# Kernel optimization log

Hardware: AMD Instinct MI355X
Metric: run time of the kernel (lower is better)

## Reference

```python
import jax, jax.numpy as jnp
import numpy as np

B, N = 512, 4
OBS, OBSU, ID = 128, 64, 16
STATE = OBS + OBSU - ID  # 176
M1, M2, G1, A = 256, 256, 256, 16
E = 128  # hypernet_embed


def setup_inputs() -> dict:
    key = jax.random.key(0)
    ks = jax.random.split(key, 24)

    def W(k, shape):
        return jax.random.normal(k, shape, dtype=jnp.float32) * 0.05

    inp = {"input": jax.random.normal(ks[0], (B, N, OBS + OBSU), dtype=jnp.float32)}
    # layer1_hypernet: Linear(ID, 10*E)
    inp["l1_W"] = W(ks[1], (10 * E, ID)); inp["l1_b"] = W(ks[2], (10 * E,))
    # hyper_net{i}_w / hyper_net{i}_b : Linear(E, in*out) / Linear(E, out)
    inp["w1W"] = W(ks[3], (STATE * M1, E)); inp["w1b"] = W(ks[4], (STATE * M1,))
    inp["b1W"] = W(ks[5], (M1, E));        inp["b1b"] = W(ks[6], (M1,))
    inp["w2W"] = W(ks[7], (M1 * M2, E));   inp["w2b"] = W(ks[8], (M1 * M2,))
    inp["b2W"] = W(ks[9], (M2, E));        inp["b2b"] = W(ks[10], (M2,))
    inp["w3W"] = W(ks[11], (M2 * M2, E));  inp["w3b"] = W(ks[12], (M2 * M2,))
    inp["b3W"] = W(ks[13], (M2, E));       inp["b3b"] = W(ks[14], (M2,))
    inp["w4W"] = W(ks[15], (M2 * G1, E));  inp["w4b"] = W(ks[16], (M2 * G1,))
    inp["b4W"] = W(ks[17], (G1, E));       inp["b4b"] = W(ks[18], (G1,))
    inp["w5W"] = W(ks[19], (G1 * A, E));   inp["w5b"] = W(ks[20], (G1 * A,))
    inp["b5W"] = W(ks[21], (A, E));        inp["b5b"] = W(ks[22], (A,))
    return inp


def reference(input, l1_W, l1_b, w1W, w1b, b1W, b1b, w2W, w2b, b2W, b2b,
              w3W, w3b, b3W, b3b, w4W, w4b, b4W, b4b, w5W, w5b, b5W, b5b):
    b, n, d = input.shape
    BN = b * n
    ids = input[..., -ID:].reshape(BN, ID)
    x = input[..., :-ID].reshape(BN, d - ID)  # [BN, STATE]
    # layer1_hypernet: ReLU(Linear(ID -> 10E))
    h = jax.nn.relu(ids @ l1_W.T + l1_b)  # [BN, 10E]
    chunk = lambda i: h[:, i * E:(i + 1) * E]

    def layer(x, iw, ib, wW, wb, bW, bb, out_dim, act):
        # generate per-sample weight [BN, in, out] and bias [BN, out]
        Wm = (chunk(iw) @ wW.T + wb).reshape(BN, x.shape[-1], out_dim)
        bm = chunk(ib) @ bW.T + bb
        y = jnp.einsum('bs,bsm->bm', x, Wm) + bm  # batched GEMV
        return jax.nn.relu(y) if act else y

    out = layer(x,   0, 1, w1W, w1b, b1W, b1b, M1, True)
    out = layer(out, 2, 3, w2W, w2b, b2W, b2b, M2, True)
    out = layer(out, 4, 5, w3W, w3b, b3W, b3b, M2, True)
    out = layer(out, 6, 7, w4W, w4b, b4W, b4b, G1, False)  # no ReLU after layer 4
    out = layer(out, 8, 9, w5W, w5b, b5W, b5b, A, True)
    return out.reshape(b, n, A)
```

## Files before the change

### kernel.cpp

```cpp
#include <hip/hip_runtime.h>
#include <hip/hip_bf16.h>

#define E_ 128
#define NSAMP 2048

typedef __attribute__((ext_vector_type(8))) short short8;
typedef __attribute__((ext_vector_type(4))) float floatx4;

__device__ __forceinline__ ushort f2b(float f) {
    union { __hip_bfloat16 h; ushort u; } cv;
    cv.h = __float2bfloat16(f);
    return cv.u;
}

__device__ __forceinline__ void gload_lds16(const ushort* g, ushort* l) {
    __builtin_amdgcn_global_load_lds(
        (const __attribute__((address_space(1))) void*)g,
        (__attribute__((address_space(3))) void*)l, 16, 0, 0);
}

__global__ void hyper_h(const float* __restrict__ input, const float* __restrict__ l1W,
                        const float* __restrict__ l1b, float* __restrict__ h)
{
    int b = blockIdx.x / 5;
    int o = (blockIdx.x % 5) * 256 + threadIdx.x;
    const float* ids = input + (size_t)b * 192 + 176;
    const float* w = l1W + (size_t)o * 16;
    float a = l1b[o];
#pragma unroll
    for (int i = 0; i < 16; i += 4) {
        float4 wv = *(const float4*)(w + i);
        a += ids[i] * wv.x + ids[i + 1] * wv.y + ids[i + 2] * wv.z + ids[i + 3] * wv.w;
    }
    h[(size_t)b * 1280 + o] = fmaxf(a, 0.f);
}

__global__ void x0_t(const float* __restrict__ input, float* __restrict__ xT0)
{
    int idx = blockIdx.x * 256 + threadIdx.x;
    int s = idx >> 11, b = idx & 2047;
    xT0[idx] = input[(size_t)b * 192 + s];
}

__global__ void cvt_layer(const float* __restrict__ wW, const float* __restrict__ wb,
                          const float* __restrict__ bW, ushort* __restrict__ dst,
                          int S, int M)
{
    int i = (blockIdx.x * 256 + threadIdx.x) * 8;
    const int nW = S * M * E_;
    union { ushort o[8]; uint4 v; } u;
    if (i < nW) {
        float4 a = *(const float4*)(wW + i);
        float4 b = *(const float4*)(wW + i + 4);
        u.o[0] = f2b(a.x); u.o[1] = f2b(a.y); u.o[2] = f2b(a.z); u.o[3] = f2b(a.w);
        u.o[4] = f2b(b.x); u.o[5] = f2b(b.y); u.o[6] = f2b(b.z); u.o[7] = f2b(b.w);
    } else {
        int rem = i - nW;
        int slice = rem / (M * E_);
        int r2 = rem - slice * (M * E_);
        int m = r2 >> 7, e = r2 & 127;
        if (slice == 0) {
            const float* src = bW + (size_t)m * E_ + e;
            float4 a = *(const float4*)(src);
            float4 b = *(const float4*)(src + 4);
            u.o[0] = f2b(a.x); u.o[1] = f2b(a.y); u.o[2] = f2b(a.z); u.o[3] = f2b(a.w);
            u.o[4] = f2b(b.x); u.o[5] = f2b(b.y); u.o[6] = f2b(b.z); u.o[7] = f2b(b.w);
        } else {
#pragma unroll
            for (int jj = 0; jj < 8; ++jj) {
                int s = (slice - 1) * 128 + e + jj;
                u.o[jj] = (s < S) ? f2b(wb[(size_t)s * M + m]) : (ushort)0;
            }
        }
    }
    *(uint4*)(dst + i) = u.v;
}

__global__ __launch_bounds__(256, 2) void gemm_big(
    const ushort* __restrict__ wWb, const float* __restrict__ h,
    const float* __restrict__ xT, float* __restrict__ partial,
    int S, int iw, int ksplit, int btiles, int ntiles)
{
    __shared__ __align__(16) ushort Bs[2][2 * 128 * 64];
    __shared__ __align__(16) float xs[17 * 128];

    const int tid = threadIdx.x;
    const int bid = blockIdx.x;
    const int xcd = bid & 7;
    const int jj_ = bid >> 3;
    const int combo = xcd + 8 * (jj_ / btiles);
    const int bt = jj_ % btiles;
    const int nt = combo % ntiles;
    const int ks = combo / ntiles;
    const int b0 = bt * 128;
    const int m0 = nt * 128;
    const int total_s = S + 3;
    const int base = total_s / ksplit;
    const int rem = total_s - base * ksplit;
    const int s0 = ks * base + min(ks, rem);
    const int s1v = s0 + base + (ks < rem ? 1 : 0);
    const int sE = min(s1v, S);
    const int ns = sE - s0;

    const int lane = tid & 63;
    const int wave = tid >> 6;
    const int quad = lane >> 4;
    const int lr = lane & 15;
    const int wm0 = wave * 32;

    const int brow = lane >> 3;
    const int bgg = (lane & 7) ^ brow;

    float hreg[2][2][2][8];
#pragma unroll
    for (int i = 0; i < 2; ++i)
#pragma unroll
        for (int p = 0; p < 2; ++p)
#pragma unroll
            for (int k2 = 0; k2 < 2; ++k2) {
                const float* src = h + (size_t)(b0 + wm0 + i * 16 + lr) * 1280
                                     + (size_t)iw * E_ + p * 64 + k2 * 32 + quad * 8;
                float4 v0 = *(const float4*)(src);
                float4 v1 = *(const float4*)(src + 4);
                hreg[i][p][k2][0] = v0.x; hreg[i][p][k2][1] = v0.y;
                hreg[i][p][k2][2] = v0.z; hreg[i][p][k2][3] = v0.w;
                hreg[i][p][k2][4] = v1.x; hreg[i][p][k2][5] = v1.y;
                hreg[i][p][k2][6] = v1.z; hreg[i][p][k2][7] = v1.w;
            }

    for (int idx = tid; idx < ns * 128; idx += 256) {
        int j = idx >> 7, bb2 = idx & 127;
        xs[idx] = xT[(size_t)(s0 + j) * NSAMP + b0 + bb2];
    }

    floatx4 acc[2][8];
#pragma unroll
    for (int i = 0; i < 2; ++i)
#pragma unroll
        for (int j = 0; j < 8; ++j)
            acc[i][j] = (floatx4){0.f, 0.f, 0.f, 0.f};

    auto dmaB = [&](int s, ushort* buf) {
#pragma unroll
        for (int p = 0; p < 2; ++p)
#pragma unroll
            for (int t4 = 0; t4 < 4; ++t4) {
                int rloc = wave * 32 + t4 * 8;
                const ushort* gp = wWb + ((size_t)s * 256 + m0 + rloc + brow) * E_ + p * 64 + bgg * 8;
                gload_lds16(gp, buf + (size_t)p * 8192 + (size_t)rloc * 64 + lane * 8);
            }
    };
    auto dmaBh = [&](int s, int p, ushort* buf) {
#pragma unroll
        for (int t4 = 0; t4 < 4; ++t4) {
            int rloc = wave * 32 + t4 * 8;
            const ushort* gp = wWb + ((size_t)s * 256 + m0 + rloc + brow) * E_ + p * 64 + bgg * 8;
            gload_lds16(gp, buf + (size_t)rloc * 64 + lane * 8);
        }
    };

    __builtin_amdgcn_sched_barrier(0);
    __syncthreads();
    __builtin_amdgcn_sched_barrier(0);
    dmaB(s0, &Bs[0][0]);
    if (ns > 1) dmaB(s0 + 1, &Bs[1][0]);

    for (int si = 0; si < ns; ++si) {
        const float xr0 = xs[si * 128 + wm0 + lr];
        const float xr1 = xs[si * 128 + wm0 + 16 + lr];
        short8 af0[2][2], af1[2][2];
#pragma unroll
        for (int p = 0; p < 2; ++p)
#pragma unroll
            for (int k2 = 0; k2 < 2; ++k2)
#pragma unroll
                for (int j = 0; j < 8; ++j) {
                    af0[p][k2][j] = (short)f2b(xr0 * hreg[0][p][k2][j]);
                    af1[p][k2][j] = (short)f2b(xr1 * hreg[1][p][k2][j]);
                }

        if (si + 1 < ns) asm volatile("s_waitcnt vmcnt(8)" ::: "memory");
        else             asm volatile("s_waitcnt vmcnt(0)" ::: "memory");
        __builtin_amdgcn_sched_barrier(0);
        __builtin_amdgcn_s_barrier();
        __builtin_amdgcn_sched_barrier(0);

        const ushort* bcur = &Bs[si & 1][0];
        __builtin_amdgcn_s_setprio(1);
#pragma unroll
        for (int kk = 0; kk < 4; ++kk) {
            const int p = kk >> 1, k2 = kk & 1;
            const int swz = ((k2 * 4 + quad) ^ (lr & 7)) * 8;
            short8 bfr[8];
#pragma unroll
            for (int j = 0; j < 8; ++j)
                bfr[j] = *(const short8*)&bcur[(size_t)p * 8192 + (size_t)(j * 16 + lr) * 64 + swz];
            const short8 a0 = (p == 0) ? ((k2 == 0) ? af0[0][0] : af0[0][1])
                                       : ((k2 == 0) ? af0[1][0] : af0[1][1]);
            const short8 a1 = (p == 0) ? ((k2 == 0) ? af1[0][0] : af1[0][1])
                                       : ((k2 == 0) ? af1[1][0] : af1[1][1]);
#pragma unroll
            for (int j = 0; j < 8; ++j) {
                acc[0][j] = __builtin_amdgcn_mfma_f32_16x16x32_bf16(a0, bfr[j], acc[0][j], 0, 0, 0);
                acc[1][j] = __builtin_amdgcn_mfma_f32_16x16x32_bf16(a1, bfr[j], acc[1][j], 0, 0, 0);
            }
        }
        __builtin_amdgcn_s_setprio(0);
        __builtin_amdgcn_sched_barrier(0);
        __builtin_amdgcn_s_barrier();
        __builtin_amdgcn_sched_barrier(0);

        if (si + 2 < ns) dmaB(s0 + si + 2, &Bs[si & 1][0]);
    }

    for (int s = sE; s < s1v; ++s) {
        for (int p = 0; p < 2; ++p) {
            __syncthreads();
            dmaBh(s, p, &Bs[0][0]);
            short8 af[2][2];
            if (s == S) {
#pragma unroll
                for (int k2 = 0; k2 < 2; ++k2)
#pragma unroll
                    for (int i = 0; i < 2; ++i) {
                        const float* src = h + (size_t)(b0 + wm0 + i * 16 + lr) * 1280
                                             + (size_t)(iw + 1) * E_ + p * 64 + k2 * 32 + quad * 8;
                        float4 v0 = *(const float4*)(src);
                        float4 v1 = *(const float4*)(src + 4);
                        af[k2][i][0] = (short)f2b(v0.x); af[k2][i][1] = (short)f2b(v0.y);
                        af[k2][i][2] = (short)f2b(v0.z); af[k2][i][3] = (short)f2b(v0.w);
                        af[k2][i][4] = (short)f2b(v1.x); af[k2][i][5] = (short)f2b(v1.y);
                        af[k2][i][6] = (short)f2b(v1.z); af[k2][i][7] = (short)f2b(v1.w);
                    }
            } else {
                const int jbase = (s - S - 1) * 128 + p * 64;
#pragma unroll
                for (int k2 = 0; k2 < 2; ++k2)
#pragma unroll
                    for (int i = 0; i < 2; ++i) {
                        const int b = b0 + wm0 + i * 16 + lr;
#pragma unroll
                        for (int jj = 0; jj < 8; ++jj) {
                            const int sp = jbase + k2 * 32 + quad * 8 + jj;
                            af[k2][i][jj] = (sp < S) ? (short)f2b(xT[(size_t)sp * NSAMP + b]) : (short)0;
                        }
                    }
            }
            __syncthreads();
#pragma unroll
            for (int k2 = 0; k2 < 2; ++k2) {
                const int swz = ((k2 * 4 + quad) ^ (lr & 7)) * 8;
                short8 bfr[8];
#pragma unroll
                for (int j = 0; j < 8; ++j)
                    bfr[j] = *(const short8*)&Bs[0][(size_t)(j * 16 + lr) * 64 + swz];
#pragma unroll
                for (int j = 0; j < 8; ++j) {
                    acc[0][j] = __builtin_amdgcn_mfma_f32_16x16x32_bf16(af[k2][0], bfr[j], acc[0][j], 0, 0, 0);
                    acc[1][j] = __builtin_amdgcn_mfma_f32_16x16x32_bf16(af[k2][1], bfr[j], acc[1][j], 0, 0, 0);
                }
            }
        }
    }

    float* dst = partial + (size_t)ks * NSAMP * 256;
#pragma unroll
    for (int i = 0; i < 2; ++i)
#pragma unroll
        for (int j = 0; j < 8; ++j)
#pragma unroll
            for (int r = 0; r < 4; ++r) {
                const int row = wm0 + i * 16 + quad * 4 + r;
                const int col = j * 16 + lr;
                dst[(size_t)(b0 + row) * 256 + m0 + col] = acc[i][j][r];
            }
}

template<int BM, int BN, int WROWS, int WCOLS>
__global__ __launch_bounds__(256, 2) void gemm_k(
    const ushort* __restrict__ wWb, const float* __restrict__ h,
    const float* __restrict__ xT, float* __restrict__ partial,
    int S, int M, int iw, int ksplit, int btiles, int ntiles)
{
    constexpr int SM = BM / WROWS / 16;
    constexpr int SN = BN / WCOLS / 16;
    constexpr int ASLOTS = BM * 8 / 256;
    constexpr int LDA = 72;

    __shared__ ushort As[BM][LDA];
    __shared__ ushort Bs[BN][LDA];

    const int tid = threadIdx.x;
    const int bt = blockIdx.x % btiles;
    const int nt = (blockIdx.x / btiles) % ntiles;
    const int ks = blockIdx.x / (btiles * ntiles);
    const int b0 = bt * BM;
    const int m0 = nt * BN;
    const int total_s = S + 3;
    const int base = total_s / ksplit;
    const int rem = total_s - base * ksplit;
    const int s0 = ks * base + min(ks, rem);
    const int s1 = s0 + base + (ks < rem ? 1 : 0);

    const int lane = tid & 63;
    const int wave = tid >> 6;
    const int quad = lane >> 4;
    const int lr = lane & 15;
    const int wm0 = (wave / WCOLS) * (BM / WROWS);
    const int wn0 = (wave % WCOLS) * (BN / WCOLS);

    const int tb = tid >> 3;
    const int teg = tid & 7;

    float hreg[ASLOTS][2][8];
#pragma unroll
    for (int k2 = 0; k2 < ASLOTS; ++k2) {
        int b = tb + 32 * k2;
#pragma unroll
        for (int p = 0; p < 2; ++p) {
            const float* src = h + (size_t)(b0 + b) * 1280 + (size_t)iw * E_ + p * 64 + teg * 8;
            float4 v0 = *(const float4*)(src);
            float4 v1 = *(const float4*)(src + 4);
            hreg[k2][p][0] = v0.x; hreg[k2][p][1] = v0.y; hreg[k2][p][2] = v0.z; hreg[k2][p][3] = v0.w;
            hreg[k2][p][4] = v1.x; hreg[k2][p][5] = v1.y; hreg[k2][p][6] = v1.z; hreg[k2][p][7] = v1.w;
        }
    }

    floatx4 acc[SM][SN];
#pragma unroll
    for (int i = 0; i < SM; ++i)
#pragma unroll
        for (int j = 0; j < SN; ++j)
            acc[i][j] = (floatx4){0.f, 0.f, 0.f, 0.f};

    for (int s = s0; s < s1; ++s) {
        float xv[ASLOTS];
        if (s < S) {
#pragma unroll
            for (int k2 = 0; k2 < ASLOTS; ++k2)
                xv[k2] = xT[(size_t)s * NSAMP + b0 + tb + 32 * k2];
        }

#pragma unroll
        for (int p = 0; p < 2; ++p) {
            if (s < S) {
#pragma unroll
                for (int k2 = 0; k2 < ASLOTS; ++k2) {
                    union { ushort o[8]; uint4 v; } u;
#pragma unroll
                    for (int j = 0; j < 8; ++j) u.o[j] = f2b(xv[k2] * hreg[k2][p][j]);
                    *(uint4*)&As[tb + 32 * k2][teg * 8] = u.v;
                }
            } else if (s == S) {
#pragma unroll
                for (int k2 = 0; k2 < ASLOTS; ++k2) {
                    const float* src = h + (size_t)(b0 + tb + 32 * k2) * 1280
                                         + (size_t)(iw + 1) * E_ + p * 64 + teg * 8;
                    float4 v0 = *(const float4*)(src);
                    float4 v1 = *(const float4*)(src + 4);
                    union { ushort o[8]; uint4 v; } u;
                    u.o[0] = f2b(v0.x); u.o[1] = f2b(v0.y); u.o[2] = f2b(v0.z); u.o[3] = f2b(v0.w);
                    u.o[4] = f2b(v1.x); u.o[5] = f2b(v1.y); u.o[6] = f2b(v1.z); u.o[7] = f2b(v1.w);
                    *(uint4*)&As[tb + 32 * k2][teg * 8] = u.v;
                }
            } else {
                int j0 = (s - S - 1) * 128 + p * 64 + teg * 8;
#pragma unroll
                for (int k2 = 0; k2 < ASLOTS; ++k2) {
                    int b = b0 + tb + 32 * k2;
                    union { ushort o[8]; uint4 v; } u;
#pragma unroll
                    for (int jj = 0; jj < 8; ++jj) {
                        int sp = j0 + jj;
                        u.o[jj] = (sp < S) ? f2b(xT[(size_t)sp * NSAMP + b]) : (ushort)0;
                    }
                    *(uint4*)&As[tb + 32 * k2][teg * 8] = u.v;
                }
            }
#pragma unroll
            for (int slot = tid; slot < BN * 8; slot += 256) {
                int m = slot >> 3, eg2 = slot & 7;
                *(uint4*)&Bs[m][eg2 * 8] =
                    *(const uint4*)(wWb + ((size_t)s * M + m0 + m) * E_ + p * 64 + eg2 * 8);
            }
            __syncthreads();
#pragma unroll
            for (int kk = 0; kk < 2; ++kk) {
                short8 af[SM], bfr[SN];
#pragma unroll
                for (int i = 0; i < SM; ++i)
                    af[i] = *(const short8*)&As[wm0 + i * 16 + lr][kk * 32 + quad * 8];
#pragma unroll
                for (int j = 0; j < SN; ++j)
                    bfr[j] = *(const short8*)&Bs[wn0 + j * 16 + lr][kk * 32 + quad * 8];
#pragma unroll
                for (int i = 0; i < SM; ++i)
#pragma unroll
                    for (int j = 0; j < SN; ++j)
                        acc[i][j] = __builtin_amdgcn_mfma_f32_16x16x32_bf16(af[i], bfr[j], acc[i][j], 0, 0, 0);
            }
            __syncthreads();
        }
    }

    float* dst = partial + (size_t)ks * NSAMP * M;
#pragma unroll
    for (int i = 0; i < SM; ++i)
#pragma unroll
        for (int j = 0; j < SN; ++j)
#pragma unroll
            for (int r = 0; r < 4; ++r) {
                int row = wm0 + i * 16 + quad * 4 + r;
                int col = wn0 + j * 16 + lr;
                dst[(size_t)(b0 + row) * M + m0 + col] = acc[i][j][r];
            }
}

__global__ void reduce_mid(const float* __restrict__ partial, const float* __restrict__ bb,
                           float* __restrict__ xTn, int KS, int relu)
{
    __shared__ float t[32][33];
    const int b0 = (blockIdx.x >> 3) * 32;
    const int m0 = (blockIdx.x & 7) * 32;
    const int mo = threadIdx.x & 31;
    const int bs0 = threadIdx.x >> 5;
    const float bv = bb[m0 + mo];
#pragma unroll
    for (int r = 0; r < 4; ++r) {
        const int bs = bs0 + 8 * r;
        const size_t off = (size_t)(b0 + bs) * 256 + m0 + mo;
        float a0 = 0.f, a1 = 0.f, a2 = 0.f, a3 = 0.f;
#pragma unroll
        for (int k = 0; k < 16; k += 4) {
            a0 += partial[(size_t)(k + 0) * (NSAMP * 256) + off];
            a1 += partial[(size_t)(k + 1) * (NSAMP * 256) + off];
            a2 += partial[(size_t)(k + 2) * (NSAMP * 256) + off];
            a3 += partial[(size_t)(k + 3) * (NSAMP * 256) + off];
        }
        float a = (a0 + a1) + (a2 + a3) + bv;
        if (relu) a = fmaxf(a, 0.f);
        t[bs][mo] = a;
    }
    __syncthreads();
    const int bo = threadIdx.x & 31;
    const int ms0 = threadIdx.x >> 5;
#pragma unroll
    for (int r = 0; r < 4; ++r) {
        const int ms = ms0 + 8 * r;
        xTn[(size_t)(m0 + ms) * NSAMP + b0 + bo] = t[bo][ms];
    }
}

__global__ void reduce_out(const float* __restrict__ partial, const float* __restrict__ bb,
                           float* __restrict__ out, int KS)
{
    int idx = blockIdx.x * 256 + threadIdx.x;
    float a0 = 0.f, a1 = 0.f, a2 = 0.f, a3 = 0.f;
#pragma unroll
    for (int k = 0; k < 64; k += 4) {
        a0 += partial[(size_t)(k + 0) * (NSAMP * 16) + idx];
        a1 += partial[(size_t)(k + 1) * (NSAMP * 16) + idx];
        a2 += partial[(size_t)(k + 2) * (NSAMP * 16) + idx];
        a3 += partial[(size_t)(k + 3) * (NSAMP * 16) + idx];
    }
    out[idx] = fmaxf((a0 + a1) + (a2 + a3) + bb[idx & 15], 0.f);
}

extern "C" void kernel_launch(void* const* d_in, const int* in_sizes, int n_in,
                              void* d_out, int out_size, void* d_ws, size_t ws_size,
                              hipStream_t stream)
{
    const float* input = (const float*)d_in[0];
    const float* l1W   = (const float*)d_in[1];
    const float* l1b   = (const float*)d_in[2];

    char* ws = (char*)d_ws;
    ushort* wWb = (ushort*)(ws + 0);
    float* h    = (float*)(ws + 16975872);
    float* xT0  = (float*)(ws + 27461632);
    float* xT1  = (float*)(ws + 29558784);
    float* part = (float*)(ws + 31655936);

    hipLaunchKernelGGL(hyper_h, dim3(2048 * 5), dim3(256), 0, stream, input, l1W, l1b, h);
    hipLaunchKernelGGL(x0_t, dim3(176 * 2048 / 256), dim3(256), 0, stream, input, xT0);

    const int S_[5] = {176, 256, 256, 256, 256};
    const int M_[5] = {256, 256, 256, 256, 16};
    float* xt[2] = {xT0, xT1};

    for (int i = 0; i < 5; ++i) {
        const float* wW = (const float*)d_in[3 + 4 * i];
        const float* wb = (const float*)d_in[4 + 4 * i];
        const float* bW = (const float*)d_in[5 + 4 * i];
        const float* bb = (const float*)d_in[6 + 4 * i];
        float* xin = xt[i & 1];
        int ntot = (S_[i] + 3) * M_[i] * E_;
        hipLaunchKernelGGL(cvt_layer, dim3(ntot / 2048), dim3(256), 0, stream,
                           wW, wb, bW, wWb, S_[i], M_[i]);

        if (M_[i] == 256) {
            const int btiles = 16, ntiles = 2, ksplit = 16;
            hipLaunchKernelGGL(gemm_big, dim3(btiles * ntiles * ksplit), dim3(256), 0, stream,
                               wWb, h, xin, part, S_[i], 2 * i, ksplit, btiles, ntiles);
            hipLaunchKernelGGL(reduce_mid, dim3(512), dim3(256), 0, stream,
                               part, bb, xt[(i + 1) & 1], ksplit, (i < 3) ? 1 : 0);
        } else {
            const int btiles = 8, ntiles = 1, ksplit = 64;
            hipLaunchKernelGGL((gemm_k<256, 16, 4, 1>), dim3(btiles * ntiles * ksplit), dim3(256), 0, stream,
                               wWb, h, xin, part, S_[i], 16, 2 * i, ksplit, btiles, ntiles);
            hipLaunchKernelGGL(reduce_out, dim3(128), dim3(256), 0, stream,
                               part, bb, (float*)d_out, ksplit);
        }
    }
}
```

Baseline: 533.1 us.

## Use 512-thread blocks with 2x2 wave tiling and triple-buffered half-step pipeline

Doubles the gemm_big block to 8 waves, splitting the 128x128 output tile 4x2 across waves so each wave holds half the accumulators. The B-tile prefetch now works on half-steps (one 64-wide K slice) through a 3-slot ring buffer, issued right after a single barrier per half-step instead of two barriers per step. A-fragment construction moves inside the half-step loop. The goal is more waves to hide latency and a finer-grained overlap of DMA with MFMA. The cost is lower MFMA work per wave relative to LDS B reads, and a higher launch-bounds occupancy target that may pressure registers.

```diff
diff --git a/kernel.cpp b/kernel.cpp
--- a/kernel.cpp
+++ b/kernel.cpp
@@ -76,12 +76,12 @@
     *(uint4*)(dst + i) = u.v;
 }
 
-__global__ __launch_bounds__(256, 2) void gemm_big(
+__global__ __launch_bounds__(512, 4) void gemm_big(
     const ushort* __restrict__ wWb, const float* __restrict__ h,
     const float* __restrict__ xT, float* __restrict__ partial,
     int S, int iw, int ksplit, int btiles, int ntiles)
 {
-    __shared__ __align__(16) ushort Bs[2][2 * 128 * 64];
+    __shared__ __align__(16) ushort Bs[3 * 128 * 64];
     __shared__ __align__(16) float xs[17 * 128];
 
     const int tid = threadIdx.x;
@@ -101,12 +101,14 @@
     const int s1v = s0 + base + (ks < rem ? 1 : 0);
     const int sE = min(s1v, S);
     const int ns = sE - s0;
+    const int T = 2 * ns;
 
     const int lane = tid & 63;
     const int wave = tid >> 6;
     const int quad = lane >> 4;
     const int lr = lane & 15;
-    const int wm0 = wave * 32;
+    const int wm0 = (wave >> 1) * 32;
+    const int wn0 = (wave & 1) * 64;
 
     const int brow = lane >> 3;
     const int bgg = (lane & 7) ^ brow;
@@ -128,32 +130,22 @@
                 hreg[i][p][k2][6] = v1.z; hreg[i][p][k2][7] = v1.w;
             }
 
-    for (int idx = tid; idx < ns * 128; idx += 256) {
+    for (int idx = tid; idx < ns * 128; idx += 512) {
         int j = idx >> 7, bb2 = idx & 127;
         xs[idx] = xT[(size_t)(s0 + j) * NSAMP + b0 + bb2];
     }
 
-    floatx4 acc[2][8];
+    floatx4 acc[2][4];
 #pragma unroll
     for (int i = 0; i < 2; ++i)
 #pragma unroll
-        for (int j = 0; j < 8; ++j)
+        for (int j = 0; j < 4; ++j)
             acc[i][j] = (floatx4){0.f, 0.f, 0.f, 0.f};
 
-    auto dmaB = [&](int s, ushort* buf) {
-#pragma unroll
-        for (int p = 0; p < 2; ++p)
-#pragma unroll
-            for (int t4 = 0; t4 < 4; ++t4) {
-                int rloc = wave * 32 + t4 * 8;
-                const ushort* gp = wWb + ((size_t)s * 256 + m0 + rloc + brow) * E_ + p * 64 + bgg * 8;
-                gload_lds16(gp, buf + (size_t)p * 8192 + (size_t)rloc * 64 + lane * 8);
-            }
-    };
-    auto dmaBh = [&](int s, int p, ushort* buf) {
-#pragma unroll
-        for (int t4 = 0; t4 < 4; ++t4) {
-            int rloc = wave * 32 + t4 * 8;
+    auto dmaP = [&](int s, int p, ushort* buf) {
+#pragma unroll
+        for (int rnd = 0; rnd < 2; ++rnd) {
+            int rloc = wave * 16 + rnd * 8;
             const ushort* gp = wWb + ((size_t)s * 256 + m0 + rloc + brow) * E_ + p * 64 + bgg * 8;
             gload_lds16(gp, buf + (size_t)rloc * 64 + lane * 8);
         }
@@ -162,61 +154,59 @@
     __builtin_amdgcn_sched_barrier(0);
     __syncthreads();
     __builtin_amdgcn_sched_barrier(0);
-    dmaB(s0, &Bs[0][0]);
-    if (ns > 1) dmaB(s0 + 1, &Bs[1][0]);
-
+    if (T > 0) dmaP(s0, 0, Bs);
+    if (T > 1) dmaP(s0, 1, Bs + 8192);
+
+    int cb = 0, rf = 2;
     for (int si = 0; si < ns; ++si) {
         const float xr0 = xs[si * 128 + wm0 + lr];
         const float xr1 = xs[si * 128 + wm0 + 16 + lr];
-        short8 af0[2][2], af1[2][2];
-#pragma unroll
-        for (int p = 0; p < 2; ++p)
-#pragma unroll
-            for (int k2 = 0; k2 < 2; ++k2)
-#pragma unroll
-                for (int j = 0; j < 8; ++j) {
-                    af0[p][k2][j] = (short)f2b(xr0 * hreg[0][p][k2][j]);
-                    af1[p][k2][j] = (short)f2b(xr1 * hreg[1][p][k2][j]);
+#pragma unroll
+        for (int P = 0; P < 2; ++P) {
+            const int t = 2 * si + P;
+            if (t + 1 < T) { asm volatile("s_waitcnt vmcnt(2)" ::: "memory"); }
+            else           { asm volatile("s_waitcnt vmcnt(0)" ::: "memory"); }
+            __builtin_amdgcn_sched_barrier(0);
+            __builtin_amdgcn_s_barrier();
+            __builtin_amdgcn_sched_barrier(0);
+
+            if (t + 2 < T) {
+                const int tn = t + 2;
+                dmaP(s0 + (tn >> 1), tn & 1, Bs + (size_t)rf * 8192);
+            }
+
+            const ushort* bcur = Bs + (size_t)cb * 8192;
+            __builtin_amdgcn_s_setprio(1);
+#pragma unroll
+            for (int k2 = 0; k2 < 2; ++k2) {
+                const int swz = ((k2 * 4 + quad) ^ (lr & 7)) * 8;
+                short8 bfr[4];
+#pragma unroll
+                for (int j = 0; j < 4; ++j)
+                    bfr[j] = *(const short8*)&bcur[(size_t)(wn0 + j * 16 + lr) * 64 + swz];
+                short8 a0, a1;
+#pragma unroll
+                for (int jj = 0; jj < 8; ++jj) {
+                    a0[jj] = (short)f2b(xr0 * hreg[0][P][k2][jj]);
+                    a1[jj] = (short)f2b(xr1 * hreg[1][P][k2][jj]);
                 }
-
-        if (si + 1 < ns) asm volatile("s_waitcnt vmcnt(8)" ::: "memory");
-        else             asm volatile("s_waitcnt vmcnt(0)" ::: "memory");
-        __builtin_amdgcn_sched_barrier(0);
-        __builtin_amdgcn_s_barrier();
-        __builtin_amdgcn_sched_barrier(0);
-
-        const ushort* bcur = &Bs[si & 1][0];
-        __builtin_amdgcn_s_setprio(1);
-#pragma unroll
-        for (int kk = 0; kk < 4; ++kk) {
-            const int p = kk >> 1, k2 = kk & 1;
-            const int swz = ((k2 * 4 + quad) ^ (lr & 7)) * 8;
-            short8 bfr[8];
-#pragma unroll
-            for (int j = 0; j < 8; ++j)
-                bfr[j] = *(const short8*)&bcur[(size_t)p * 8192 + (size_t)(j * 16 + lr) * 64 + swz];
-            const short8 a0 = (p == 0) ? ((k2 == 0) ? af0[0][0] : af0[0][1])
-                                       : ((k2 == 0) ? af0[1][0] : af0[1][1]);
-            const short8 a1 = (p == 0) ? ((k2 == 0) ? af1[0][0] : af1[0][1])
-                                       : ((k2 == 0) ? af1[1][0] : af1[1][1]);
-#pragma unroll
-            for (int j = 0; j < 8; ++j) {
-                acc[0][j] = __builtin_amdgcn_mfma_f32_16x16x32_bf16(a0, bfr[j], acc[0][j], 0, 0, 0);
-                acc[1][j] = __builtin_amdgcn_mfma_f32_16x16x32_bf16(a1, bfr[j], acc[1][j], 0, 0, 0);
-            }
-        }
-        __builtin_amdgcn_s_setprio(0);
-        __builtin_amdgcn_sched_barrier(0);
-        __builtin_amdgcn_s_barrier();
-        __builtin_amdgcn_sched_barrier(0);
-
-        if (si + 2 < ns) dmaB(s0 + si + 2, &Bs[si & 1][0]);
+#pragma unroll
+                for (int j = 0; j < 4; ++j) {
+                    acc[0][j] = __builtin_amdgcn_mfma_f32_16x16x32_bf16(a0, bfr[j], acc[0][j], 0, 0, 0);
+                    acc[1][j] = __builtin_amdgcn_mfma_f32_16x16x32_bf16(a1, bfr[j], acc[1][j], 0, 0, 0);
+                }
+            }
+            __builtin_amdgcn_s_setprio(0);
+
+            cb = (cb + 1 == 3) ? 0 : cb + 1;
+            rf = (rf + 1 == 3) ? 0 : rf + 1;
+        }
     }
 
     for (int s = sE; s < s1v; ++s) {
         for (int p = 0; p < 2; ++p) {
             __syncthreads();
-            dmaBh(s, p, &Bs[0][0]);
+            dmaP(s, p, Bs);
             short8 af[2][2];
             if (s == S) {
 #pragma unroll
@@ -250,12 +240,12 @@
 #pragma unroll
             for (int k2 = 0; k2 < 2; ++k2) {
                 const int swz = ((k2 * 4 + quad) ^ (lr & 7)) * 8;
-                short8 bfr[8];
-#pragma unroll
-                for (int j = 0; j < 8; ++j)
-                    bfr[j] = *(const short8*)&Bs[0][(size_t)(j * 16 + lr) * 64 + swz];
-#pragma unroll
-                for (int j = 0; j < 8; ++j) {
+                short8 bfr[4];
+#pragma unroll
+                for (int j = 0; j < 4; ++j)
+                    bfr[j] = *(const short8*)&Bs[(size_t)(wn0 + j * 16 + lr) * 64 + swz];
+#pragma unroll
+                for (int j = 0; j < 4; ++j) {
                     acc[0][j] = __builtin_amdgcn_mfma_f32_16x16x32_bf16(af[k2][0], bfr[j], acc[0][j], 0, 0, 0);
                     acc[1][j] = __builtin_amdgcn_mfma_f32_16x16x32_bf16(af[k2][1], bfr[j], acc[1][j], 0, 0, 0);
                 }
@@ -267,11 +257,11 @@
 #pragma unroll
     for (int i = 0; i < 2; ++i)
 #pragma unroll
-        for (int j = 0; j < 8; ++j)
+        for (int j = 0; j < 4; ++j)
 #pragma unroll
             for (int r = 0; r < 4; ++r) {
                 const int row = wm0 + i * 16 + quad * 4 + r;
-                const int col = j * 16 + lr;
+                const int col = wn0 + j * 16 + lr;
                 dst[(size_t)(b0 + row) * 256 + m0 + col] = acc[i][j][r];
             }
 }
@@ -500,7 +490,7 @@
 
         if (M_[i] == 256) {
             const int btiles = 16, ntiles = 2, ksplit = 16;
-            hipLaunchKernelGGL(gemm_big, dim3(btiles * ntiles * ksplit), dim3(256), 0, stream,
+            hipLaunchKernelGGL(gemm_big, dim3(btiles * ntiles * ksplit), dim3(512), 0, stream,
                                wWb, h, xin, part, S_[i], 2 * i, ksplit, btiles, ntiles);
             hipLaunchKernelGGL(reduce_mid, dim3(512), dim3(256), 0, stream,
                                part, bb, xt[(i + 1) & 1], ksplit, (i < 3) ? 1 : 0);
```

Result: slower. 636.8 us (+19.4%).
